# Kernel tuning notes

Measured on AMD Instinct MI355X. Metric: run time of the kernel, lower is better.

## Reference

```python
import jax, jax.numpy as jnp
import numpy as np

# Static model config (matches init_kwargs)
B, N, L, S = 128, 5, 128, 8   # batch, n_vars, n_lags, patch_size
P = L // S                    # n_patches = 16
D = 64                        # d_hidden
DT = 16                       # d_time
DIN = DT + 1                  # TTCN input dim (time embed + value)
NF = D - 1                    # TTCN output channels (d_hidden - 1)
DG = 16                       # d_graph
NH = 4                        # n_heads
GNN_L = 2                     # gnn_layers
NB = 2                        # n_blocks
NC = 39                       # n_classes


def _time_embed(t, omega, alpha):
    # t: (...,) -> (..., DT); channel 0 linear, rest sinusoidal (Eq. 3)
    lin = omega[0] * t + alpha[0]
    per = jnp.sin(omega[1:] * t[..., None] + alpha[1:])
    return jnp.concatenate([lin[..., None], per], axis=-1)


def _ln(x, g, b, eps=1e-5):
    mu = x.mean(-1, keepdims=True)
    v = ((x - mu) ** 2).mean(-1, keepdims=True)
    return (x - mu) * jax.lax.rsqrt(v + eps) * g + b


def _mha(x, wi, bi, wo, bo):
    # torch nn.MultiheadAttention (batch_first) self-attention, no mask
    Bq, Pq, Dq = x.shape
    dh = Dq // NH
    qkv = x @ wi.T + bi
    q, k, v = jnp.split(qkv, 3, axis=-1)
    sp = lambda a: a.reshape(Bq, Pq, NH, dh).transpose(0, 2, 1, 3)
    q, k, v = sp(q), sp(k), sp(v)
    scale = 1.0 / np.sqrt(dh)
    a = jax.nn.softmax(jnp.einsum('bhqd,bhkd->bhqk', q, k) * scale, axis=-1)
    o = jnp.einsum('bhqk,bhkd->bhqd', a, v).transpose(0, 2, 1, 3).reshape(Bq, Pq, Dq)
    return o @ wo.T + bo


def _ttcn(z, mask, w1, b1, w2, b2):
    # z: (T,S,DIN); vectorizes torch's per-output-channel loop over NF filters
    h = jax.nn.relu(jnp.einsum('tsi,fji->tfsj', z, w1) + b1[:, None, :])
    lg = jnp.einsum('tfsj,fkj->tfsk', h, w2) + b2[:, None, :]
    lg = jnp.where(mask[:, None, :, None], lg, -1e9)
    w = jax.nn.softmax(lg, axis=2)  # softmax over patch-length dim
    return jnp.einsum('tfsi,tsi->tf', w, z)  # (weights*z).sum(s).sum(i)


def _block(h, p):
    (wi, bi, wo, bo, g1, be1, fw1, fb1, fw2, fb2, g2, be2,
     Es1, Es2, Wd1, bd1, Wd2, bd2, Wg1, bg1, Wg2, bg2, gW, gb, g3, be3) = p
    Bh = h.shape[0]
    # intra-series transformer over patches
    x = h.reshape(Bh * N, P, D)
    x = _ln(x + _mha(x, wi, bi, wo, bo), g1, be1)
    x = _ln(x + (jax.nn.relu(x @ fw1.T + fb1) @ fw2.T + fb2), g2, be2)
    # inter-series GSL + GNN, vectorized over the per-patch python loop
    hh = x.reshape(Bh, N, P, D).transpose(0, 2, 1, 3).reshape(Bh * P, N, D)
    Es1b = jnp.broadcast_to(Es1, (Bh * P, N, DG))
    Es2b = jnp.broadcast_to(Es2, (Bh * P, N, DG))
    Ed1 = hh @ Wd1.T + bd1
    gg1 = jax.nn.relu(jnp.tanh(jnp.concatenate([hh, Es1b], -1) @ Wg1.T + bg1))
    Ep1 = Es1b + gg1 * Ed1
    Ed2 = hh @ Wd2.T + bd2
    gg2 = jax.nn.relu(jnp.tanh(jnp.concatenate([hh, Es2b], -1) @ Wg2.T + bg2))
    Ep2 = Es2b + gg2 * Ed2
    A = jax.nn.softmax(jax.nn.relu(jnp.einsum('bnd,bmd->bnm', Ep1, Ep2)), axis=-1)
    res = hh @ gW[0].T + gb[0]
    Ap = A
    for m in range(1, GNN_L + 1):
        res = res + (Ap @ hh) @ gW[m].T + gb[m]
        if m < GNN_L:
            Ap = Ap @ A
    hg = jax.nn.relu(res)
    out = _ln(hh + hg, g3, be3)
    return out.reshape(Bh, P, N, D).transpose(0, 2, 1, 3)


def setup_inputs():
    key = jax.random.key(0)
    ks = iter(jax.random.split(key, 64))
    rn = lambda *s: jax.random.normal(next(ks), s, dtype=jnp.float32)
    d = {}
    d['x'] = rn(B, N, L)
    d['t_rel'] = jnp.broadcast_to(jnp.arange(L, dtype=jnp.float32), (B, L)) * 1.0
    d['te_omega'] = rn(DT); d['te_alpha'] = rn(DT)
    d['mf_w1'] = rn(NF, DIN, DIN) * 0.1; d['mf_b1'] = rn(NF, DIN) * 0.02
    d['mf_w2'] = rn(NF, DIN, DIN) * 0.1; d['mf_b2'] = rn(NF, DIN) * 0.02
    d['pos_enc'] = rn(1, 1, P, D) * 0.02
    d['attn_in_w'] = rn(NB, 3 * D, D) * 0.05; d['attn_in_b'] = rn(NB, 3 * D) * 0.02
    d['attn_out_w'] = rn(NB, D, D) * 0.05; d['attn_out_b'] = rn(NB, D) * 0.02
    d['ln1_g'] = jnp.ones((NB, D)); d['ln1_b'] = jnp.zeros((NB, D))
    d['ffn_w1'] = rn(NB, 2 * D, D) * 0.05; d['ffn_b1'] = rn(NB, 2 * D) * 0.02
    d['ffn_w2'] = rn(NB, D, 2 * D) * 0.05; d['ffn_b2'] = rn(NB, D) * 0.02
    d['ln2_g'] = jnp.ones((NB, D)); d['ln2_b'] = jnp.zeros((NB, D))
    d['gsl_Es1'] = rn(NB, N, DG); d['gsl_Es2'] = rn(NB, N, DG)
    d['gsl_Wd1'] = rn(NB, DG, D) * 0.05; d['gsl_bd1'] = rn(NB, DG) * 0.02
    d['gsl_Wd2'] = rn(NB, DG, D) * 0.05; d['gsl_bd2'] = rn(NB, DG) * 0.02
    d['gsl_Wg1'] = rn(NB, 1, D + DG) * 0.05; d['gsl_bg1'] = rn(NB, 1) * 0.02
    d['gsl_Wg2'] = rn(NB, 1, D + DG) * 0.05; d['gsl_bg2'] = rn(NB, 1) * 0.02
    d['gnn_W'] = rn(NB, GNN_L + 1, D, D) * 0.05; d['gnn_b'] = rn(NB, GNN_L + 1, D) * 0.02
    d['ln3_g'] = jnp.ones((NB, D)); d['ln3_b'] = jnp.zeros((NB, D))
    d['fp_w'] = rn(D, P * D) * 0.02; d['fp_b'] = rn(D) * 0.02
    d['q_omega'] = rn(DT); d['q_alpha'] = rn(DT)
    d['ow1'] = rn(N, D, D + DT) * 0.05; d['ob1'] = rn(N, D) * 0.02
    d['ow2'] = rn(N, D, D) * 0.05; d['ob2'] = rn(N, D) * 0.02
    d['ow3'] = rn(N, NC, D) * 0.05; d['ob3'] = rn(N, NC) * 0.02
    return d


def reference(x, t_rel, te_omega, te_alpha, mf_w1, mf_b1, mf_w2, mf_b2, pos_enc,
              attn_in_w, attn_in_b, attn_out_w, attn_out_b, ln1_g, ln1_b,
              ffn_w1, ffn_b1, ffn_w2, ffn_b2, ln2_g, ln2_b,
              gsl_Es1, gsl_Es2, gsl_Wd1, gsl_bd1, gsl_Wd2, gsl_bd2,
              gsl_Wg1, gsl_bg1, gsl_Wg2, gsl_bg2, gnn_W, gnn_b, ln3_g, ln3_b,
              fp_w, fp_b, q_omega, q_alpha, ow1, ob1, ow2, ob2, ow3, ob3):
    # patching: L divisible by S -> no padding, mask all True
    v = x.reshape(B, N, P, S)
    t = jnp.broadcast_to(t_rel.reshape(B, 1, P, S), (B, N, P, S)).reshape(-1, S)
    mask = jnp.ones((B * N * P, S), dtype=bool)
    te = _time_embed(t, te_omega, te_alpha)               # (T,S,DT)
    z = jnp.concatenate([te, v.reshape(-1, S)[..., None]], -1)  # (T,S,DIN)
    hc = _ttcn(z, mask, mf_w1, mf_b1, mf_w2, mf_b2)       # (T,NF)
    mp = mask.any(1).astype(z.dtype)[:, None]
    h = jnp.concatenate([hc, mp], -1).reshape(B, N, P, D) + pos_enc
    for bk in range(NB):
        p = (attn_in_w[bk], attn_in_b[bk], attn_out_w[bk], attn_out_b[bk],
             ln1_g[bk], ln1_b[bk], ffn_w1[bk], ffn_b1[bk], ffn_w2[bk], ffn_b2[bk],
             ln2_g[bk], ln2_b[bk], gsl_Es1[bk], gsl_Es2[bk], gsl_Wd1[bk], gsl_bd1[bk],
             gsl_Wd2[bk], gsl_bd2[bk], gsl_Wg1[bk], gsl_bg1[bk], gsl_Wg2[bk], gsl_bg2[bk],
             gnn_W[bk], gnn_b[bk], ln3_g[bk], ln3_b[bk])
        h = _block(h, p)
    flat = h.reshape(B, N, P * D)
    Hf = flat @ fp_w.T + fp_b                              # (B,N,D)
    q = _time_embed(jnp.full((B,), float(L), dtype=x.dtype), q_omega, q_alpha)
    inp = jnp.concatenate([Hf, jnp.broadcast_to(q[:, None, :], (B, N, DT))], -1)
    h1 = jax.nn.relu(jnp.einsum('bni,noi->bno', inp, ow1) + ob1)
    h2 = jax.nn.relu(jnp.einsum('bni,noi->bno', h1, ow2) + ob2)
    return jnp.einsum('bni,noi->bno', h2, ow3) + ob3       # (B,N,NC) raw logits
```

## Files before the change

kernel.cpp:

```cpp
#include <hip/hip_runtime.h>
#include <math.h>

#define CB 128
#define CN 5
#define CL 128
#define CS 8
#define CP 16
#define CD 64
#define CDT 16
#define CDIN 17
#define CNF 63
#define CNC 39

__device__ __forceinline__ float wave_sum(float v) {
    v += __shfl_xor(v, 32);
    v += __shfl_xor(v, 16);
    v += __shfl_xor(v, 8);
    v += __shfl_xor(v, 4);
    v += __shfl_xor(v, 2);
    v += __shfl_xor(v, 1);
    return v;
}

__global__ void prep_kernel(
    const float* __restrict__ mf_w1, const float* __restrict__ mf_w2,
    const float* __restrict__ mf_b2, const float* __restrict__ fp_w,
    const float* __restrict__ attn_in_w, const float* __restrict__ attn_out_w,
    const float* __restrict__ ffn_w1, const float* __restrict__ ffn_w2,
    const float* __restrict__ gnn_W, const float* __restrict__ gsl_Wd1,
    const float* __restrict__ gsl_Wd2,
    const float* __restrict__ ow1, const float* __restrict__ ow2,
    const float* __restrict__ ow3,
    float* __restrict__ w1c16, float* __restrict__ w2t, float* __restrict__ b2t,
    float* __restrict__ fp_wt, float* __restrict__ wit, float* __restrict__ wot,
    float* __restrict__ fw1t, float* __restrict__ fw2t,
    float* __restrict__ gWt, float* __restrict__ Wd1t, float* __restrict__ Wd2t,
    float* __restrict__ o1t, float* __restrict__ o2t, float* __restrict__ o3t) {
    int idx = blockIdx.x * 256 + threadIdx.x;
    if (idx < 65536) {
        int d = idx >> 10, j = idx & 1023;
        fp_wt[j * 64 + d] = fp_w[idx];
    }
    if (idx < 18496) {
        int f = idx / 289, rem = idx % 289;
        w2t[rem * 64 + f] = (f < CNF) ? mf_w2[idx] : 0.f;
    }
    if (idx < 1088) {
        int f = idx / 17, r = idx % 17;
        b2t[r * 64 + f]   = (f < CNF) ? mf_b2[idx] : 0.f;
        w1c16[r * 64 + f] = (f < CNF) ? mf_w1[idx * 17 + 16] : 0.f;
    }
    if (idx < 24576) {
        int bk = idx / 12288, rem = idx % 12288;
        int oc = rem >> 6, d = rem & 63;
        wit[bk * 12288 + d * 192 + oc] = attn_in_w[idx];
    }
    if (idx < 8192) {
        int bk = idx >> 12, rem = idx & 4095;
        int d = rem >> 6, c = rem & 63;
        wot[bk * 4096 + c * 64 + d] = attn_out_w[idx];
    }
    if (idx < 16384) {
        int bk = idx >> 13, rem = idx & 8191;
        int c = rem >> 6, d = rem & 63;
        fw1t[bk * 8192 + d * 128 + c] = ffn_w1[idx];
    }
    if (idx < 16384) {
        int bk = idx >> 13, rem = idx & 8191;
        int d = rem >> 7, c = rem & 127;
        fw2t[bk * 8192 + c * 64 + d] = ffn_w2[idx];
    }
    if (idx < 24576) {
        int bk = idx / 12288, rem = idx % 12288;
        int m = rem >> 12, r2 = rem & 4095;
        int o = r2 >> 6, c = r2 & 63;
        gWt[bk * 12288 + m * 4096 + c * 64 + o] = gnn_W[idx];
    }
    if (idx < 2048) {
        int bk = idx >> 10, rem = idx & 1023;
        int l = rem >> 6, d = rem & 63;
        Wd1t[bk * 1024 + d * 16 + l] = gsl_Wd1[idx];
        Wd2t[bk * 1024 + d * 16 + l] = gsl_Wd2[idx];
    }
    if (idx < 25600) {
        int n = idx / 5120, rem = idx % 5120;
        int o = rem / 80, i = rem % 80;
        o1t[n * 5120 + i * 64 + o] = ow1[idx];
    }
    if (idx < 20480) {
        int n = idx >> 12, rem = idx & 4095;
        int o = rem >> 6, i = rem & 63;
        o2t[n * 4096 + i * 64 + o] = ow2[idx];
    }
    if (idx < 12480) {
        int n = idx / 2496, rem = idx % 2496;
        int o = rem >> 6, i = rem & 63;
        o3t[n * 4096 + i * 64 + o] = ow3[idx];
    }
}

__global__ __launch_bounds__(64) void prep2_kernel(
    const float* __restrict__ t_rel, const float* __restrict__ omega, const float* __restrict__ alpha,
    const float* __restrict__ mf_w1, const float* __restrict__ mf_b1,
    float* __restrict__ base, float* __restrict__ te_tab) {
    const int blk = blockIdx.x;
    const int j = blk % 17;
    const int ps = blk / 17;
    const int p = ps >> 3, s = ps & 7;
    const int f = threadIdx.x;

    const float t = t_rel[p * CS + s];
    float te[16];
#pragma unroll
    for (int i = 0; i < 16; ++i)
        te[i] = (i == 0) ? (omega[0] * t + alpha[0]) : sinf(omega[i] * t + alpha[i]);

    float acc = 0.f;
    if (f < CNF) {
        acc = mf_b1[f * 17 + j];
        const float* w = mf_w1 + (f * 17 + j) * 17;
#pragma unroll
        for (int i = 0; i < 16; ++i) acc = fmaf(te[i], w[i], acc);
    }
    base[((p * 17 + j) * 8 + s) * 64 + f] = acc;

    if (j == 0 && f < 16) te_tab[ps * 16 + f] = te[f];
}

template <int K0, int KC>
__device__ __forceinline__ float ttcn_chunk(
    const float* __restrict__ w2t, const float* bse, const float* w1c,
    const float* b2s, const float* tes, const float v_s[8], int lane) {
    float lg[KC][8];
#pragma unroll
    for (int kk = 0; kk < KC; ++kk) {
        float bb = b2s[(K0 + kk) * 64 + lane];
#pragma unroll
        for (int s = 0; s < 8; ++s) lg[kk][s] = bb;
    }
#pragma unroll 1
    for (int j = 0; j < 17; ++j) {
        float w1 = w1c[j * 64 + lane];
        float h_s[8];
#pragma unroll
        for (int s = 0; s < 8; ++s)
            h_s[s] = fmaxf(fmaf(v_s[s], w1, bse[(j * 8 + s) * 64 + lane]), 0.f);
#pragma unroll
        for (int kk = 0; kk < KC; ++kk) {
            float w2 = w2t[((K0 + kk) * 17 + j) * 64 + lane];
#pragma unroll
            for (int s = 0; s < 8; ++s) lg[kk][s] = fmaf(h_s[s], w2, lg[kk][s]);
        }
    }
    float out = 0.f;
#pragma unroll
    for (int kk = 0; kk < KC; ++kk) {
        const int k = K0 + kk;
        float m = lg[kk][0];
#pragma unroll
        for (int s = 1; s < 8; ++s) m = fmaxf(m, lg[kk][s]);
        float l = 0.f, o = 0.f;
#pragma unroll
        for (int s = 0; s < 8; ++s) {
            float e = __expf(lg[kk][s] - m);
            l += e;
            o = fmaf(e, (k < 16) ? tes[s * 16 + k] : v_s[s], o);
        }
        out += o / l;
    }
    return out;
}

__global__ __launch_bounds__(512, 2) void ttcn_kernel(
    const float* __restrict__ x, const float* __restrict__ base,
    const float* __restrict__ te_tab, const float* __restrict__ w1c16,
    const float* __restrict__ w2t, const float* __restrict__ b2t,
    const float* __restrict__ pos_enc, float* __restrict__ hout) {
    __shared__ float bse[8704];
    __shared__ float w1c[1088];
    __shared__ float b2s[1088];
    __shared__ float tes[128];
    const int tid = threadIdx.x;
    const int p = blockIdx.x / 80, g = blockIdx.x % 80;

    {
        const float4* bsrc4 = (const float4*)(base + p * 8704);
        float4* bse4 = (float4*)bse;
        for (int i = tid; i < 2176; i += 512) bse4[i] = bsrc4[i];
        const float4* w1c4 = (const float4*)w1c16;
        const float4* b2t4 = (const float4*)b2t;
        float4* dw = (float4*)w1c;
        float4* db = (float4*)b2s;
        if (tid < 272) { dw[tid] = w1c4[tid]; db[tid] = b2t4[tid]; }
        if (tid < 128) tes[tid] = te_tab[p * 128 + tid];
    }
    __syncthreads();

    const int wid = tid >> 6, lane = tid & 63;
    const int bn = g * 8 + wid;
    const int tok = bn * 16 + p;

    float v_s[8];
    {
        const float4* xv = (const float4*)(x + tok * 8);
        float4 x0 = xv[0], x1 = xv[1];
        v_s[0] = x0.x; v_s[1] = x0.y; v_s[2] = x0.z; v_s[3] = x0.w;
        v_s[4] = x1.x; v_s[5] = x1.y; v_s[6] = x1.z; v_s[7] = x1.w;
    }

    float out = 0.f;
    out += ttcn_chunk<0, 5>(w2t, bse, w1c, b2s, tes, v_s, lane);
    out += ttcn_chunk<5, 4>(w2t, bse, w1c, b2s, tes, v_s, lane);
    out += ttcn_chunk<9, 4>(w2t, bse, w1c, b2s, tes, v_s, lane);
    out += ttcn_chunk<13, 4>(w2t, bse, w1c, b2s, tes, v_s, lane);

    float val = (lane < CNF) ? out : 1.0f;
    hout[tok * 64 + lane] = val + pos_enc[p * 64 + lane];
}

__global__ __launch_bounds__(256) void intra_kernel(
    float* __restrict__ h,
    const float* __restrict__ wit, const float* __restrict__ bi,
    const float* __restrict__ wot, const float* __restrict__ bo,
    const float* __restrict__ g1, const float* __restrict__ be1,
    const float* __restrict__ fw1t, const float* __restrict__ fb1,
    const float* __restrict__ fw2t, const float* __restrict__ fb2,
    const float* __restrict__ g2, const float* __restrict__ be2) {
    __shared__ float xs[16][64];
    __shared__ float qs[16][64];
    __shared__ float ks[16][64];
    __shared__ float vs[16][64];
    __shared__ float sc[4][16][16];
    __shared__ float os[16][64];
    __shared__ float x1[16][64];
    __shared__ float fs[16][128];

    const int row = blockIdx.x;
    float* xin = h + row * CP * CD;
    const int t = threadIdx.x;

    for (int e = t; e < 1024; e += 256) xs[e >> 6][e & 63] = xin[e];
    __syncthreads();

    if (t < 192) {
        const int oc = t;
        float acc[16];
#pragma unroll
        for (int p = 0; p < 16; ++p) acc[p] = bi[oc];
        for (int d = 0; d < 64; ++d) {
            float w = wit[d * 192 + oc];
#pragma unroll
            for (int p = 0; p < 16; ++p) acc[p] = fmaf(xs[p][d], w, acc[p]);
        }
#pragma unroll
        for (int p = 0; p < 16; ++p) {
            if (oc < 64)       qs[p][oc] = acc[p];
            else if (oc < 128) ks[p][oc - 64] = acc[p];
            else               vs[p][oc - 128] = acc[p];
        }
    }
    __syncthreads();

    for (int e = t; e < 1024; e += 256) {
        int hh = e >> 8, i = (e >> 4) & 15, j = e & 15;
        float acc = 0.f;
        for (int d = 0; d < 16; ++d) acc = fmaf(qs[i][hh * 16 + d], ks[j][hh * 16 + d], acc);
        sc[hh][i][j] = acc * 0.25f;
    }
    __syncthreads();

    if (t < 64) {
        int hh = t >> 4, i = t & 15;
        float m = sc[hh][i][0];
#pragma unroll
        for (int j = 1; j < 16; ++j) m = fmaxf(m, sc[hh][i][j]);
        float e_[16];
        float l = 0.f;
#pragma unroll
        for (int j = 0; j < 16; ++j) { e_[j] = __expf(sc[hh][i][j] - m); l += e_[j]; }
        float inv = 1.f / l;
#pragma unroll
        for (int j = 0; j < 16; ++j) sc[hh][i][j] = e_[j] * inv;
    }
    __syncthreads();

    for (int e = t; e < 1024; e += 256) {
        int p = e >> 6, c = e & 63, hh = c >> 4;
        float acc = 0.f;
        for (int j = 0; j < 16; ++j) acc = fmaf(sc[hh][p][j], vs[j][c], acc);
        os[p][c] = acc;
    }
    __syncthreads();

    for (int e = t; e < 1024; e += 256) {
        int p = e >> 6, d = e & 63;
        float acc = bo[d];
        for (int c = 0; c < 64; ++c) acc = fmaf(os[p][c], wot[c * 64 + d], acc);
        x1[p][d] = acc + xs[p][d];
    }
    __syncthreads();

    {
        int w = t >> 6, lane = t & 63;
        for (int p = w; p < 16; p += 4) {
            float v = x1[p][lane];
            float mu = wave_sum(v) * (1.f / 64);
            float d = v - mu;
            float var = wave_sum(d * d) * (1.f / 64);
            x1[p][lane] = d * rsqrtf(var + 1e-5f) * g1[lane] + be1[lane];
        }
    }
    __syncthreads();

    for (int e = t; e < 2048; e += 256) {
        int p = e >> 7, c = e & 127;
        float acc = fb1[c];
        for (int d = 0; d < 64; ++d) acc = fmaf(x1[p][d], fw1t[d * 128 + c], acc);
        fs[p][c] = fmaxf(acc, 0.f);
    }
    __syncthreads();

    for (int e = t; e < 1024; e += 256) {
        int p = e >> 6, d = e & 63;
        float acc = fb2[d];
        for (int c = 0; c < 128; ++c) acc = fmaf(fs[p][c], fw2t[c * 64 + d], acc);
        os[p][d] = acc + x1[p][d];
    }
    __syncthreads();

    {
        int w = t >> 6, lane = t & 63;
        for (int p = w; p < 16; p += 4) {
            float v = os[p][lane];
            float mu = wave_sum(v) * (1.f / 64);
            float d = v - mu;
            float var = wave_sum(d * d) * (1.f / 64);
            xin[p * 64 + lane] = d * rsqrtf(var + 1e-5f) * g2[lane] + be2[lane];
        }
    }
}

__global__ __launch_bounds__(320) void gnn_kernel(
    float* __restrict__ h,
    const float* __restrict__ Es1, const float* __restrict__ Es2,
    const float* __restrict__ Wd1t, const float* __restrict__ bd1,
    const float* __restrict__ Wd2t, const float* __restrict__ bd2,
    const float* __restrict__ Wg1, const float* __restrict__ bg1,
    const float* __restrict__ Wg2, const float* __restrict__ bg2,
    const float* __restrict__ gWt, const float* __restrict__ gb,
    const float* __restrict__ g3, const float* __restrict__ be3) {
    __shared__ float hs[5][64];
    __shared__ float ep1[5][16], ep2[5][16];
    __shared__ float Araw[5][8], As[5][8], A2s[5][8];
    __shared__ float t1s[5][64], t2s[5][64];

    const int bp = blockIdx.x;
    const int b = bp >> 4, p = bp & 15;
    const int n = threadIdx.x >> 6, lane = threadIdx.x & 63;
    float* hptr = h + (((b * CN + n) * CP + p) * CD);

    hs[n][lane] = hptr[lane];
    __syncthreads();

    float a1 = 0.f, a2 = 0.f;
    if (lane < 16) {
        a1 = bd1[lane]; a2 = bd2[lane];
        for (int d = 0; d < 64; ++d) {
            a1 = fmaf(hs[n][d], Wd1t[d * 16 + lane], a1);
            a2 = fmaf(hs[n][d], Wd2t[d * 16 + lane], a2);
        }
    }
    float p1 = hs[n][lane] * Wg1[lane] + ((lane < 16) ? Es1[n * 16 + lane] * Wg1[64 + lane] : 0.f);
    float p2 = hs[n][lane] * Wg2[lane] + ((lane < 16) ? Es2[n * 16 + lane] * Wg2[64 + lane] : 0.f);
    float gg1 = fmaxf(tanhf(wave_sum(p1) + bg1[0]), 0.f);
    float gg2 = fmaxf(tanhf(wave_sum(p2) + bg2[0]), 0.f);
    if (lane < 16) {
        ep1[n][lane] = Es1[n * 16 + lane] + gg1 * a1;
        ep2[n][lane] = Es2[n * 16 + lane] + gg2 * a2;
    }
    __syncthreads();

    if (lane < 5) {
        float e = 0.f;
#pragma unroll
        for (int k = 0; k < 16; ++k) e = fmaf(ep1[n][k], ep2[lane][k], e);
        Araw[n][lane] = fmaxf(e, 0.f);
    }
    __syncthreads();
    if (lane < 5) {
        float m = Araw[n][0];
#pragma unroll
        for (int j = 1; j < 5; ++j) m = fmaxf(m, Araw[n][j]);
        float l = 0.f;
#pragma unroll
        for (int j = 0; j < 5; ++j) l += __expf(Araw[n][j] - m);
        As[n][lane] = __expf(Araw[n][lane] - m) / l;
    }
    __syncthreads();
    if (lane < 5) {
        float a = 0.f;
#pragma unroll
        for (int l2 = 0; l2 < 5; ++l2) a = fmaf(As[n][l2], As[l2][lane], a);
        A2s[n][lane] = a;
    }
    __syncthreads();

    {
        float t1 = 0.f, t2 = 0.f;
#pragma unroll
        for (int m = 0; m < 5; ++m) {
            t1 = fmaf(As[n][m], hs[m][lane], t1);
            t2 = fmaf(A2s[n][m], hs[m][lane], t2);
        }
        t1s[n][lane] = t1;
        t2s[n][lane] = t2;
    }
    __syncthreads();

    float res = gb[lane] + gb[64 + lane] + gb[128 + lane];
    for (int c = 0; c < 64; ++c) {
        res = fmaf(hs[n][c], gWt[c * 64 + lane], res);
        res = fmaf(t1s[n][c], gWt[4096 + c * 64 + lane], res);
        res = fmaf(t2s[n][c], gWt[8192 + c * 64 + lane], res);
    }
    float pre = hs[n][lane] + fmaxf(res, 0.f);

    float mu = wave_sum(pre) * (1.f / 64);
    float d = pre - mu;
    float var = wave_sum(d * d) * (1.f / 64);
    hptr[lane] = d * rsqrtf(var + 1e-5f) * g3[lane] + be3[lane];
}

__global__ __launch_bounds__(256) void head_kernel(
    const float* __restrict__ h, const float* __restrict__ fp_wt, const float* __restrict__ fp_b,
    const float* __restrict__ q_omega, const float* __restrict__ q_alpha,
    const float* __restrict__ o1t, const float* __restrict__ ob1,
    const float* __restrict__ o2t, const float* __restrict__ ob2,
    const float* __restrict__ o3t, const float* __restrict__ ob3,
    float* __restrict__ out) {
    __shared__ float flat[1024];
    __shared__ float part[4][64];
    __shared__ float inp[80];
    __shared__ float h1s[64], h2s[64];
    const int row = blockIdx.x;
    const int n = row % CN;
    const int t = threadIdx.x, wid = t >> 6, lane = t & 63;
    const float* src = h + row * CP * CD;

    for (int e = t; e < 1024; e += 256) flat[e] = src[e];
    __syncthreads();

    float a0 = 0.f, a1 = 0.f, a2 = 0.f, a3 = 0.f;
    const int j0 = wid * 256;
    for (int j = 0; j < 256; j += 4) {
        a0 = fmaf(flat[j0 + j],     fp_wt[(j0 + j) * 64 + lane],     a0);
        a1 = fmaf(flat[j0 + j + 1], fp_wt[(j0 + j + 1) * 64 + lane], a1);
        a2 = fmaf(flat[j0 + j + 2], fp_wt[(j0 + j + 2) * 64 + lane], a2);
        a3 = fmaf(flat[j0 + j + 3], fp_wt[(j0 + j + 3) * 64 + lane], a3);
    }
    part[wid][lane] = (a0 + a1) + (a2 + a3);
    if (t >= 64 && t < 80) {
        int i = t - 64;
        const float tt = (float)CL;
        inp[64 + i] = (i == 0) ? (q_omega[0] * tt + q_alpha[0])
                               : sinf(q_omega[i] * tt + q_alpha[i]);
    }
    __syncthreads();
    if (t < 64) inp[t] = fp_b[t] + ((part[0][t] + part[1][t]) + (part[2][t] + part[3][t]));
    __syncthreads();

    if (t < 64) {
        float a = ob1[n * 64 + t];
        for (int i = 0; i < 80; ++i) a = fmaf(inp[i], o1t[n * 5120 + i * 64 + t], a);
        h1s[t] = fmaxf(a, 0.f);
    }
    __syncthreads();
    if (t < 64) {
        float a = ob2[n * 64 + t];
        for (int i = 0; i < 64; ++i) a = fmaf(h1s[i], o2t[n * 4096 + i * 64 + t], a);
        h2s[t] = fmaxf(a, 0.f);
    }
    __syncthreads();
    if (t < CNC) {
        float a = ob3[n * CNC + t];
        for (int i = 0; i < 64; ++i) a = fmaf(h2s[i], o3t[n * 4096 + i * 64 + t], a);
        out[row * CNC + t] = a;
    }
}

extern "C" void kernel_launch(void* const* d_in, const int* in_sizes, int n_in,
                              void* d_out, int out_size, void* d_ws, size_t ws_size,
                              hipStream_t stream) {
    const float* x         = (const float*)d_in[0];
    const float* t_rel     = (const float*)d_in[1];
    const float* te_omega  = (const float*)d_in[2];
    const float* te_alpha  = (const float*)d_in[3];
    const float* mf_w1     = (const float*)d_in[4];
    const float* mf_b1     = (const float*)d_in[5];
    const float* mf_w2     = (const float*)d_in[6];
    const float* mf_b2     = (const float*)d_in[7];
    const float* pos_enc   = (const float*)d_in[8];
    const float* attn_in_w = (const float*)d_in[9];
    const float* attn_in_b = (const float*)d_in[10];
    const float* attn_out_w= (const float*)d_in[11];
    const float* attn_out_b= (const float*)d_in[12];
    const float* ln1_g     = (const float*)d_in[13];
    const float* ln1_b     = (const float*)d_in[14];
    const float* ffn_w1    = (const float*)d_in[15];
    const float* ffn_b1    = (const float*)d_in[16];
    const float* ffn_w2    = (const float*)d_in[17];
    const float* ffn_b2    = (const float*)d_in[18];
    const float* ln2_g     = (const float*)d_in[19];
    const float* ln2_b     = (const float*)d_in[20];
    const float* gsl_Es1   = (const float*)d_in[21];
    const float* gsl_Es2   = (const float*)d_in[22];
    const float* gsl_Wd1   = (const float*)d_in[23];
    const float* gsl_bd1   = (const float*)d_in[24];
    const float* gsl_Wd2   = (const float*)d_in[25];
    const float* gsl_bd2   = (const float*)d_in[26];
    const float* gsl_Wg1   = (const float*)d_in[27];
    const float* gsl_bg1   = (const float*)d_in[28];
    const float* gsl_Wg2   = (const float*)d_in[29];
    const float* gsl_bg2   = (const float*)d_in[30];
    const float* gnn_W     = (const float*)d_in[31];
    const float* gnn_b     = (const float*)d_in[32];
    const float* ln3_g     = (const float*)d_in[33];
    const float* ln3_b     = (const float*)d_in[34];
    const float* fp_w      = (const float*)d_in[35];
    const float* fp_b      = (const float*)d_in[36];
    const float* q_omega   = (const float*)d_in[37];
    const float* q_alpha   = (const float*)d_in[38];
    const float* ow1       = (const float*)d_in[39];
    const float* ob1       = (const float*)d_in[40];
    const float* ow2       = (const float*)d_in[41];
    const float* ob2       = (const float*)d_in[42];
    const float* ow3       = (const float*)d_in[43];
    const float* ob3       = (const float*)d_in[44];

    float* ws = (float*)d_ws;
    float* hbuf   = ws;
    float* base   = hbuf + 655360;
    float* te_tab = base + 139264;
    float* w1c16  = te_tab + 2048;
    float* w2t    = w1c16 + 1088;
    float* b2t    = w2t + 18496;
    float* fp_wt  = b2t + 1088;
    float* wit    = fp_wt + 65536;
    float* wot    = wit + 24576;
    float* fw1t   = wot + 8192;
    float* fw2t   = fw1t + 16384;
    float* gWt    = fw2t + 16384;
    float* Wd1t   = gWt + 24576;
    float* Wd2t   = Wd1t + 2048;
    float* o1t    = Wd2t + 2048;
    float* o2t    = o1t + 25600;
    float* o3t    = o2t + 20480;

    prep_kernel<<<256, 256, 0, stream>>>(
        mf_w1, mf_w2, mf_b2, fp_w, attn_in_w, attn_out_w, ffn_w1, ffn_w2,
        gnn_W, gsl_Wd1, gsl_Wd2, ow1, ow2, ow3,
        w1c16, w2t, b2t, fp_wt, wit, wot, fw1t, fw2t, gWt, Wd1t, Wd2t,
        o1t, o2t, o3t);

    prep2_kernel<<<CP * CS * CDIN, 64, 0, stream>>>(t_rel, te_omega, te_alpha,
                                                    mf_w1, mf_b1, base, te_tab);

    ttcn_kernel<<<1280, 512, 0, stream>>>(x, base, te_tab, w1c16,
                                          w2t, b2t, pos_enc, hbuf);

    for (int bk = 0; bk < 2; ++bk) {
        intra_kernel<<<CB * CN, 256, 0, stream>>>(
            hbuf,
            wit + bk * 12288, attn_in_b + bk * 192,
            wot + bk * 4096, attn_out_b + bk * 64,
            ln1_g + bk * 64, ln1_b + bk * 64,
            fw1t + bk * 8192, ffn_b1 + bk * 128,
            fw2t + bk * 8192, ffn_b2 + bk * 64,
            ln2_g + bk * 64, ln2_b + bk * 64);

        gnn_kernel<<<CB * CP, 320, 0, stream>>>(
            hbuf,
            gsl_Es1 + bk * CN * 16, gsl_Es2 + bk * CN * 16,
            Wd1t + bk * 1024, gsl_bd1 + bk * 16,
            Wd2t + bk * 1024, gsl_bd2 + bk * 16,
            gsl_Wg1 + bk * 80, gsl_bg1 + bk,
            gsl_Wg2 + bk * 80, gsl_bg2 + bk,
            gWt + bk * 12288, gnn_b + bk * 3 * 64,
            ln3_g + bk * 64, ln3_b + bk * 64);
    }

    head_kernel<<<CB * CN, 256, 0, stream>>>(hbuf, fp_wt, fp_b, q_omega, q_alpha,
                                             o1t, ob1, o2t, ob2, o3t, ob3,
                                             (float*)d_out);
}
```

Measured before the change: 463.2 us.

## Interleave weights in float4 groups and drop TTCN shared-memory staging

Prep now writes every transposed weight matrix interleaved in groups of four along the reduction dimension. The intra, gnn and head kernels can then read weights and shared activations as float4 and accumulate with a dot4 helper, cutting load instruction count. The TTCN kernel no longer stages base, w1c and b2 tables into shared memory and reads them from global memory through cache instead. It also shrinks blocks to 256 threads and regroups the output channels into two larger chunks. Larger chunks raise register pressure, and global reads in TTCN may be slower than LDS if the cache does not hold the tables.

```diff
diff --git a/kernel.cpp b/kernel.cpp
--- a/kernel.cpp
+++ b/kernel.cpp
@@ -22,6 +22,14 @@
     return v;
 }
 
+__device__ __forceinline__ float dot4(float4 a, float4 b, float acc) {
+    acc = fmaf(a.x, b.x, acc);
+    acc = fmaf(a.y, b.y, acc);
+    acc = fmaf(a.z, b.z, acc);
+    acc = fmaf(a.w, b.w, acc);
+    return acc;
+}
+
 __global__ void prep_kernel(
     const float* __restrict__ mf_w1, const float* __restrict__ mf_w2,
     const float* __restrict__ mf_b2, const float* __restrict__ fp_w,
@@ -32,14 +40,14 @@
     const float* __restrict__ ow1, const float* __restrict__ ow2,
     const float* __restrict__ ow3,
     float* __restrict__ w1c16, float* __restrict__ w2t, float* __restrict__ b2t,
-    float* __restrict__ fp_wt, float* __restrict__ wit, float* __restrict__ wot,
-    float* __restrict__ fw1t, float* __restrict__ fw2t,
-    float* __restrict__ gWt, float* __restrict__ Wd1t, float* __restrict__ Wd2t,
-    float* __restrict__ o1t, float* __restrict__ o2t, float* __restrict__ o3t) {
+    float* __restrict__ fpv, float* __restrict__ witv, float* __restrict__ wotv,
+    float* __restrict__ fw1v, float* __restrict__ fw2v,
+    float* __restrict__ gWv, float* __restrict__ Wd1v, float* __restrict__ Wd2v,
+    float* __restrict__ o1v, float* __restrict__ o2v, float* __restrict__ o3v) {
     int idx = blockIdx.x * 256 + threadIdx.x;
     if (idx < 65536) {
         int d = idx >> 10, j = idx & 1023;
-        fp_wt[j * 64 + d] = fp_w[idx];
+        fpv[((j >> 2) * 64 + d) * 4 + (j & 3)] = fp_w[idx];
     }
     if (idx < 18496) {
         int f = idx / 289, rem = idx % 289;
@@ -53,49 +61,49 @@
     if (idx < 24576) {
         int bk = idx / 12288, rem = idx % 12288;
         int oc = rem >> 6, d = rem & 63;
-        wit[bk * 12288 + d * 192 + oc] = attn_in_w[idx];
+        witv[bk * 12288 + ((d >> 2) * 192 + oc) * 4 + (d & 3)] = attn_in_w[idx];
     }
     if (idx < 8192) {
         int bk = idx >> 12, rem = idx & 4095;
         int d = rem >> 6, c = rem & 63;
-        wot[bk * 4096 + c * 64 + d] = attn_out_w[idx];
+        wotv[bk * 4096 + ((c >> 2) * 64 + d) * 4 + (c & 3)] = attn_out_w[idx];
     }
     if (idx < 16384) {
         int bk = idx >> 13, rem = idx & 8191;
         int c = rem >> 6, d = rem & 63;
-        fw1t[bk * 8192 + d * 128 + c] = ffn_w1[idx];
+        fw1v[bk * 8192 + ((d >> 2) * 128 + c) * 4 + (d & 3)] = ffn_w1[idx];
     }
     if (idx < 16384) {
         int bk = idx >> 13, rem = idx & 8191;
         int d = rem >> 7, c = rem & 127;
-        fw2t[bk * 8192 + c * 64 + d] = ffn_w2[idx];
+        fw2v[bk * 8192 + ((c >> 2) * 64 + d) * 4 + (c & 3)] = ffn_w2[idx];
     }
     if (idx < 24576) {
         int bk = idx / 12288, rem = idx % 12288;
         int m = rem >> 12, r2 = rem & 4095;
         int o = r2 >> 6, c = r2 & 63;
-        gWt[bk * 12288 + m * 4096 + c * 64 + o] = gnn_W[idx];
+        gWv[bk * 12288 + m * 4096 + ((c >> 2) * 64 + o) * 4 + (c & 3)] = gnn_W[idx];
     }
     if (idx < 2048) {
         int bk = idx >> 10, rem = idx & 1023;
         int l = rem >> 6, d = rem & 63;
-        Wd1t[bk * 1024 + d * 16 + l] = gsl_Wd1[idx];
-        Wd2t[bk * 1024 + d * 16 + l] = gsl_Wd2[idx];
+        Wd1v[bk * 1024 + ((d >> 2) * 16 + l) * 4 + (d & 3)] = gsl_Wd1[idx];
+        Wd2v[bk * 1024 + ((d >> 2) * 16 + l) * 4 + (d & 3)] = gsl_Wd2[idx];
     }
     if (idx < 25600) {
         int n = idx / 5120, rem = idx % 5120;
         int o = rem / 80, i = rem % 80;
-        o1t[n * 5120 + i * 64 + o] = ow1[idx];
+        o1v[n * 5120 + ((i >> 2) * 64 + o) * 4 + (i & 3)] = ow1[idx];
     }
     if (idx < 20480) {
         int n = idx >> 12, rem = idx & 4095;
         int o = rem >> 6, i = rem & 63;
-        o2t[n * 4096 + i * 64 + o] = ow2[idx];
+        o2v[n * 4096 + ((i >> 2) * 64 + o) * 4 + (i & 3)] = ow2[idx];
     }
     if (idx < 12480) {
         int n = idx / 2496, rem = idx % 2496;
         int o = rem >> 6, i = rem & 63;
-        o3t[n * 4096 + i * 64 + o] = ow3[idx];
+        o3v[n * 4096 + ((i >> 2) * 64 + o) * 4 + (i & 3)] = ow3[idx];
     }
 }
 
@@ -129,12 +137,13 @@
 
 template <int K0, int KC>
 __device__ __forceinline__ float ttcn_chunk(
-    const float* __restrict__ w2t, const float* bse, const float* w1c,
-    const float* b2s, const float* tes, const float v_s[8], int lane) {
+    const float* __restrict__ w2t, const float* __restrict__ bse,
+    const float* __restrict__ w1c, const float* __restrict__ b2t,
+    const float* __restrict__ tes, const float v_s[8], int lane) {
     float lg[KC][8];
 #pragma unroll
     for (int kk = 0; kk < KC; ++kk) {
-        float bb = b2s[(K0 + kk) * 64 + lane];
+        float bb = b2t[(K0 + kk) * 64 + lane];
 #pragma unroll
         for (int s = 0; s < 8; ++s) lg[kk][s] = bb;
     }
@@ -171,34 +180,18 @@
     return out;
 }
 
-__global__ __launch_bounds__(512, 2) void ttcn_kernel(
+__global__ __launch_bounds__(256, 2) void ttcn_kernel(
     const float* __restrict__ x, const float* __restrict__ base,
     const float* __restrict__ te_tab, const float* __restrict__ w1c16,
     const float* __restrict__ w2t, const float* __restrict__ b2t,
     const float* __restrict__ pos_enc, float* __restrict__ hout) {
-    __shared__ float bse[8704];
-    __shared__ float w1c[1088];
-    __shared__ float b2s[1088];
-    __shared__ float tes[128];
-    const int tid = threadIdx.x;
-    const int p = blockIdx.x / 80, g = blockIdx.x % 80;
-
-    {
-        const float4* bsrc4 = (const float4*)(base + p * 8704);
-        float4* bse4 = (float4*)bse;
-        for (int i = tid; i < 2176; i += 512) bse4[i] = bsrc4[i];
-        const float4* w1c4 = (const float4*)w1c16;
-        const float4* b2t4 = (const float4*)b2t;
-        float4* dw = (float4*)w1c;
-        float4* db = (float4*)b2s;
-        if (tid < 272) { dw[tid] = w1c4[tid]; db[tid] = b2t4[tid]; }
-        if (tid < 128) tes[tid] = te_tab[p * 128 + tid];
-    }
-    __syncthreads();
-
-    const int wid = tid >> 6, lane = tid & 63;
-    const int bn = g * 8 + wid;
+    const int tid = threadIdx.x, wid = tid >> 6, lane = tid & 63;
+    const int p = blockIdx.x / 160, g = blockIdx.x % 160;
+    const int bn = g * 4 + wid;
     const int tok = bn * 16 + p;
+
+    const float* bse = base + p * 8704;
+    const float* tes = te_tab + p * 128;
 
     float v_s[8];
     {
@@ -209,10 +202,8 @@
     }
 
     float out = 0.f;
-    out += ttcn_chunk<0, 5>(w2t, bse, w1c, b2s, tes, v_s, lane);
-    out += ttcn_chunk<5, 4>(w2t, bse, w1c, b2s, tes, v_s, lane);
-    out += ttcn_chunk<9, 4>(w2t, bse, w1c, b2s, tes, v_s, lane);
-    out += ttcn_chunk<13, 4>(w2t, bse, w1c, b2s, tes, v_s, lane);
+    out += ttcn_chunk<0, 9>(w2t, bse, w1c16, b2t, tes, v_s, lane);
+    out += ttcn_chunk<9, 8>(w2t, bse, w1c16, b2t, tes, v_s, lane);
 
     float val = (lane < CNF) ? out : 1.0f;
     hout[tok * 64 + lane] = val + pos_enc[p * 64 + lane];
@@ -220,26 +211,35 @@
 
 __global__ __launch_bounds__(256) void intra_kernel(
     float* __restrict__ h,
-    const float* __restrict__ wit, const float* __restrict__ bi,
-    const float* __restrict__ wot, const float* __restrict__ bo,
+    const float* __restrict__ witv, const float* __restrict__ bi,
+    const float* __restrict__ wotv, const float* __restrict__ bo,
     const float* __restrict__ g1, const float* __restrict__ be1,
-    const float* __restrict__ fw1t, const float* __restrict__ fb1,
-    const float* __restrict__ fw2t, const float* __restrict__ fb2,
+    const float* __restrict__ fw1v, const float* __restrict__ fb1,
+    const float* __restrict__ fw2v, const float* __restrict__ fb2,
     const float* __restrict__ g2, const float* __restrict__ be2) {
-    __shared__ float xs[16][64];
-    __shared__ float qs[16][64];
-    __shared__ float ks[16][64];
-    __shared__ float vs[16][64];
-    __shared__ float sc[4][16][16];
-    __shared__ float os[16][64];
-    __shared__ float x1[16][64];
-    __shared__ float fs[16][128];
+    __shared__ __align__(16) float xs[16][64];
+    __shared__ __align__(16) float qs[16][64];
+    __shared__ __align__(16) float ks[16][64];
+    __shared__ __align__(16) float vs[16][64];
+    __shared__ __align__(16) float sc[4][16][16];
+    __shared__ __align__(16) float os[16][64];
+    __shared__ __align__(16) float x1[16][64];
+    __shared__ __align__(16) float fs[16][128];
 
     const int row = blockIdx.x;
     float* xin = h + row * CP * CD;
     const int t = threadIdx.x;
 
-    for (int e = t; e < 1024; e += 256) xs[e >> 6][e & 63] = xin[e];
+    const float4* witv4 = (const float4*)witv;
+    const float4* wotv4 = (const float4*)wotv;
+    const float4* fw1v4 = (const float4*)fw1v;
+    const float4* fw2v4 = (const float4*)fw2v;
+
+    {
+        float4* xs4 = (float4*)&xs[0][0];
+        const float4* xin4 = (const float4*)xin;
+        if (t < 256) xs4[t] = xin4[t];
+    }
     __syncthreads();
 
     if (t < 192) {
@@ -247,10 +247,11 @@
         float acc[16];
 #pragma unroll
         for (int p = 0; p < 16; ++p) acc[p] = bi[oc];
-        for (int d = 0; d < 64; ++d) {
-            float w = wit[d * 192 + oc];
-#pragma unroll
-            for (int p = 0; p < 16; ++p) acc[p] = fmaf(xs[p][d], w, acc[p]);
+        const float4* xs4 = (const float4*)&xs[0][0];
+        for (int d4 = 0; d4 < 16; ++d4) {
+            float4 wv = witv4[d4 * 192 + oc];
+#pragma unroll
+            for (int p = 0; p < 16; ++p) acc[p] = dot4(xs4[p * 16 + d4], wv, acc[p]);
         }
 #pragma unroll
         for (int p = 0; p < 16; ++p) {
@@ -263,8 +264,11 @@
 
     for (int e = t; e < 1024; e += 256) {
         int hh = e >> 8, i = (e >> 4) & 15, j = e & 15;
+        const float4* q4 = (const float4*)&qs[i][hh * 16];
+        const float4* k4 = (const float4*)&ks[j][hh * 16];
         float acc = 0.f;
-        for (int d = 0; d < 16; ++d) acc = fmaf(qs[i][hh * 16 + d], ks[j][hh * 16 + d], acc);
+#pragma unroll
+        for (int d4 = 0; d4 < 4; ++d4) acc = dot4(q4[d4], k4[d4], acc);
         sc[hh][i][j] = acc * 0.25f;
     }
     __syncthreads();
@@ -286,16 +290,26 @@
 
     for (int e = t; e < 1024; e += 256) {
         int p = e >> 6, c = e & 63, hh = c >> 4;
+        const float4* s4 = (const float4*)&sc[hh][p][0];
         float acc = 0.f;
-        for (int j = 0; j < 16; ++j) acc = fmaf(sc[hh][p][j], vs[j][c], acc);
+#pragma unroll
+        for (int j4 = 0; j4 < 4; ++j4) {
+            float4 sv = s4[j4];
+            acc = fmaf(sv.x, vs[j4 * 4 + 0][c], acc);
+            acc = fmaf(sv.y, vs[j4 * 4 + 1][c], acc);
+            acc = fmaf(sv.z, vs[j4 * 4 + 2][c], acc);
+            acc = fmaf(sv.w, vs[j4 * 4 + 3][c], acc);
+        }
         os[p][c] = acc;
     }
     __syncthreads();
 
     for (int e = t; e < 1024; e += 256) {
         int p = e >> 6, d = e & 63;
+        const float4* os4 = (const float4*)&os[p][0];
         float acc = bo[d];
-        for (int c = 0; c < 64; ++c) acc = fmaf(os[p][c], wot[c * 64 + d], acc);
+#pragma unroll
+        for (int c4 = 0; c4 < 16; ++c4) acc = dot4(os4[c4], wotv4[c4 * 64 + d], acc);
         x1[p][d] = acc + xs[p][d];
     }
     __syncthreads();
@@ -314,16 +328,20 @@
 
     for (int e = t; e < 2048; e += 256) {
         int p = e >> 7, c = e & 127;
+        const float4* x14 = (const float4*)&x1[p][0];
         float acc = fb1[c];
-        for (int d = 0; d < 64; ++d) acc = fmaf(x1[p][d], fw1t[d * 128 + c], acc);
+#pragma unroll
+        for (int d4 = 0; d4 < 16; ++d4) acc = dot4(x14[d4], fw1v4[d4 * 128 + c], acc);
         fs[p][c] = fmaxf(acc, 0.f);
     }
     __syncthreads();
 
     for (int e = t; e < 1024; e += 256) {
         int p = e >> 6, d = e & 63;
+        const float4* fs4 = (const float4*)&fs[p][0];
         float acc = fb2[d];
-        for (int c = 0; c < 128; ++c) acc = fmaf(fs[p][c], fw2t[c * 64 + d], acc);
+#pragma unroll
+        for (int c4 = 0; c4 < 32; ++c4) acc = dot4(fs4[c4], fw2v4[c4 * 64 + d], acc);
         os[p][d] = acc + x1[p][d];
     }
     __syncthreads();
@@ -343,31 +361,38 @@
 __global__ __launch_bounds__(320) void gnn_kernel(
     float* __restrict__ h,
     const float* __restrict__ Es1, const float* __restrict__ Es2,
-    const float* __restrict__ Wd1t, const float* __restrict__ bd1,
-    const float* __restrict__ Wd2t, const float* __restrict__ bd2,
+    const float* __restrict__ Wd1v, const float* __restrict__ bd1,
+    const float* __restrict__ Wd2v, const float* __restrict__ bd2,
     const float* __restrict__ Wg1, const float* __restrict__ bg1,
     const float* __restrict__ Wg2, const float* __restrict__ bg2,
-    const float* __restrict__ gWt, const float* __restrict__ gb,
+    const float* __restrict__ gWv, const float* __restrict__ gb,
     const float* __restrict__ g3, const float* __restrict__ be3) {
-    __shared__ float hs[5][64];
+    __shared__ __align__(16) float hs[5][64];
+    __shared__ __align__(16) float t1s[5][64], t2s[5][64];
     __shared__ float ep1[5][16], ep2[5][16];
     __shared__ float Araw[5][8], As[5][8], A2s[5][8];
-    __shared__ float t1s[5][64], t2s[5][64];
 
     const int bp = blockIdx.x;
     const int b = bp >> 4, p = bp & 15;
     const int n = threadIdx.x >> 6, lane = threadIdx.x & 63;
     float* hptr = h + (((b * CN + n) * CP + p) * CD);
 
+    const float4* Wd1v4 = (const float4*)Wd1v;
+    const float4* Wd2v4 = (const float4*)Wd2v;
+    const float4* gWv4  = (const float4*)gWv;
+
     hs[n][lane] = hptr[lane];
     __syncthreads();
 
     float a1 = 0.f, a2 = 0.f;
     if (lane < 16) {
         a1 = bd1[lane]; a2 = bd2[lane];
-        for (int d = 0; d < 64; ++d) {
-            a1 = fmaf(hs[n][d], Wd1t[d * 16 + lane], a1);
-            a2 = fmaf(hs[n][d], Wd2t[d * 16 + lane], a2);
+        const float4* hs4 = (const float4*)&hs[n][0];
+#pragma unroll
+        for (int d4 = 0; d4 < 16; ++d4) {
+            float4 hv = hs4[d4];
+            a1 = dot4(hv, Wd1v4[d4 * 16 + lane], a1);
+            a2 = dot4(hv, Wd2v4[d4 * 16 + lane], a2);
         }
     }
     float p1 = hs[n][lane] * Wg1[lane] + ((lane < 16) ? Es1[n * 16 + lane] * Wg1[64 + lane] : 0.f);
@@ -418,10 +443,16 @@
     __syncthreads();
 
     float res = gb[lane] + gb[64 + lane] + gb[128 + lane];
-    for (int c = 0; c < 64; ++c) {
-        res = fmaf(hs[n][c], gWt[c * 64 + lane], res);
-        res = fmaf(t1s[n][c], gWt[4096 + c * 64 + lane], res);
-        res = fmaf(t2s[n][c], gWt[8192 + c * 64 + lane], res);
+    {
+        const float4* hs4 = (const float4*)&hs[n][0];
+        const float4* t14 = (const float4*)&t1s[n][0];
+        const float4* t24 = (const float4*)&t2s[n][0];
+#pragma unroll
+        for (int c4 = 0; c4 < 16; ++c4) {
+            res = dot4(hs4[c4], gWv4[c4 * 64 + lane], res);
+            res = dot4(t14[c4], gWv4[1024 + c4 * 64 + lane], res);
+            res = dot4(t24[c4], gWv4[2048 + c4 * 64 + lane], res);
+        }
     }
     float pre = hs[n][lane] + fmaxf(res, 0.f);
 
@@ -432,33 +463,41 @@
 }
 
 __global__ __launch_bounds__(256) void head_kernel(
-    const float* __restrict__ h, const float* __restrict__ fp_wt, const float* __restrict__ fp_b,
+    const float* __restrict__ h, const float* __restrict__ fpv, const float* __restrict__ fp_b,
     const float* __restrict__ q_omega, const float* __restrict__ q_alpha,
-    const float* __restrict__ o1t, const float* __restrict__ ob1,
-    const float* __restrict__ o2t, const float* __restrict__ ob2,
-    const float* __restrict__ o3t, const float* __restrict__ ob3,
+    const float* __restrict__ o1v, const float* __restrict__ ob1,
+    const float* __restrict__ o2v, const float* __restrict__ ob2,
+    const float* __restrict__ o3v, const float* __restrict__ ob3,
     float* __restrict__ out) {
-    __shared__ float flat[1024];
+    __shared__ __align__(16) float flat[1024];
+    __shared__ __align__(16) float inp[80];
+    __shared__ __align__(16) float h1s[64], h2s[64];
     __shared__ float part[4][64];
-    __shared__ float inp[80];
-    __shared__ float h1s[64], h2s[64];
     const int row = blockIdx.x;
     const int n = row % CN;
     const int t = threadIdx.x, wid = t >> 6, lane = t & 63;
     const float* src = h + row * CP * CD;
 
-    for (int e = t; e < 1024; e += 256) flat[e] = src[e];
-    __syncthreads();
-
-    float a0 = 0.f, a1 = 0.f, a2 = 0.f, a3 = 0.f;
-    const int j0 = wid * 256;
-    for (int j = 0; j < 256; j += 4) {
-        a0 = fmaf(flat[j0 + j],     fp_wt[(j0 + j) * 64 + lane],     a0);
-        a1 = fmaf(flat[j0 + j + 1], fp_wt[(j0 + j + 1) * 64 + lane], a1);
-        a2 = fmaf(flat[j0 + j + 2], fp_wt[(j0 + j + 2) * 64 + lane], a2);
-        a3 = fmaf(flat[j0 + j + 3], fp_wt[(j0 + j + 3) * 64 + lane], a3);
-    }
-    part[wid][lane] = (a0 + a1) + (a2 + a3);
+    const float4* fpv4 = (const float4*)fpv;
+    const float4* o1v4 = (const float4*)o1v;
+    const float4* o2v4 = (const float4*)o2v;
+    const float4* o3v4 = (const float4*)o3v;
+
+    {
+        float4* flat4 = (float4*)flat;
+        const float4* src4 = (const float4*)src;
+        if (t < 256) flat4[t] = src4[t];
+    }
+    __syncthreads();
+
+    {
+        const float4* flat4 = (const float4*)flat;
+        float a0 = 0.f;
+        const int j40 = wid * 64;
+        for (int j4 = 0; j4 < 64; ++j4)
+            a0 = dot4(flat4[j40 + j4], fpv4[(j40 + j4) * 64 + lane], a0);
+        part[wid][lane] = a0;
+    }
     if (t >= 64 && t < 80) {
         int i = t - 64;
         const float tt = (float)CL;
@@ -470,20 +509,26 @@
     __syncthreads();
 
     if (t < 64) {
+        const float4* inp4 = (const float4*)inp;
         float a = ob1[n * 64 + t];
-        for (int i = 0; i < 80; ++i) a = fmaf(inp[i], o1t[n * 5120 + i * 64 + t], a);
+#pragma unroll
+        for (int i4 = 0; i4 < 20; ++i4) a = dot4(inp4[i4], o1v4[n * 1280 + i4 * 64 + t], a);
         h1s[t] = fmaxf(a, 0.f);
     }
     __syncthreads();
     if (t < 64) {
+        const float4* h14 = (const float4*)h1s;
         float a = ob2[n * 64 + t];
-        for (int i = 0; i < 64; ++i) a = fmaf(h1s[i], o2t[n * 4096 + i * 64 + t], a);
+#pragma unroll
+        for (int i4 = 0; i4 < 16; ++i4) a = dot4(h14[i4], o2v4[n * 1024 + i4 * 64 + t], a);
         h2s[t] = fmaxf(a, 0.f);
     }
     __syncthreads();
     if (t < CNC) {
+        const float4* h24 = (const float4*)h2s;
         float a = ob3[n * CNC + t];
-        for (int i = 0; i < 64; ++i) a = fmaf(h2s[i], o3t[n * 4096 + i * 64 + t], a);
+#pragma unroll
+        for (int i4 = 0; i4 < 16; ++i4) a = dot4(h24[i4], o3v4[n * 1024 + i4 * 64 + t], a);
         out[row * CNC + t] = a;
     }
 }
@@ -544,52 +589,52 @@
     float* w1c16  = te_tab + 2048;
     float* w2t    = w1c16 + 1088;
     float* b2t    = w2t + 18496;
-    float* fp_wt  = b2t + 1088;
-    float* wit    = fp_wt + 65536;
-    float* wot    = wit + 24576;
-    float* fw1t   = wot + 8192;
-    float* fw2t   = fw1t + 16384;
-    float* gWt    = fw2t + 16384;
-    float* Wd1t   = gWt + 24576;
-    float* Wd2t   = Wd1t + 2048;
-    float* o1t    = Wd2t + 2048;
-    float* o2t    = o1t + 25600;
-    float* o3t    = o2t + 20480;
+    float* fpv    = b2t + 1088;
+    float* witv   = fpv + 65536;
+    float* wotv   = witv + 24576;
+    float* fw1v   = wotv + 8192;
+    float* fw2v   = fw1v + 16384;
+    float* gWv    = fw2v + 16384;
+    float* Wd1v   = gWv + 24576;
+    float* Wd2v   = Wd1v + 2048;
+    float* o1v    = Wd2v + 2048;
+    float* o2v    = o1v + 25600;
+    float* o3v    = o2v + 20480;
 
     prep_kernel<<<256, 256, 0, stream>>>(
         mf_w1, mf_w2, mf_b2, fp_w, attn_in_w, attn_out_w, ffn_w1, ffn_w2,
         gnn_W, gsl_Wd1, gsl_Wd2, ow1, ow2, ow3,
-        w1c16, w2t, b2t, fp_wt, wit, wot, fw1t, fw2t, gWt, Wd1t, Wd2t,
-        o1t, o2t, o3t);
+        w1c16, w2t, b2t, fpv, witv, wotv, fw1v, fw2v, gWv, Wd1v, Wd2v,
+        o1v, o2v, o3v);
 
     prep2_kernel<<<CP * CS * CDIN, 64, 0, stream>>>(t_rel, te_omega, te_alpha,
                                                     mf_w1, mf_b1, base, te_tab);
 
-    ttcn_kernel<<<1280, 512, 0, stream>>>(x, base, te_tab, w1c16,
-                                          w2t, b2t, pos_enc, hbuf);
+    ttcn_kernel<<<CP * 160, 256, 0, stream>>>(x, base, te_tab, w1c16,
+                                              w2t, b2t, pos_enc, hbuf);
 
     for (int bk = 0; bk < 2; ++bk) {
         intra_kernel<<<CB * CN, 256, 0, stream>>>(
             hbuf,
-            wit + bk * 12288, attn_in_b + bk * 192,
-            wot + bk * 4096, attn_out_b + bk * 64,
+            witv + bk * 12288, attn_in_b + bk * 192,
+            wotv + bk * 4096, attn_out_b + bk * 64,
             ln1_g + bk * 64, ln1_b + bk * 64,
-            fw1t + bk * 8192, ffn_b1 + bk * 128,
-            fw2t + bk * 8192, ffn_b2 + bk * 64,
+            fw1v + bk * 8192, ffn_b1 + bk * 128,
+            fw2v + bk * 8192, ffn_b2 + bk * 64,
             ln2_g + bk * 64, ln2_b + bk * 64);
 
         gnn_kernel<<<CB * CP, 320, 0, stream>>>(
             hbuf,
             gsl_Es1 + bk * CN * 16, gsl_Es2 + bk * CN * 16,
-            Wd1t + bk * 1024, gsl_bd1 + bk * 16,
-            Wd2t + bk * 1024, gsl_bd2 + bk * 16,
+            Wd1v + bk * 1024, gsl_bd1 + bk * 16,
+            Wd2v + bk * 1024, gsl_bd2 + bk * 16,
             gsl_Wg1 + bk * 80, gsl_bg1 + bk,
             gsl_Wg2 + bk * 80, gsl_bg2 + bk,
-            gWt + bk * 12288, gnn_b + bk * 3 * 64,
+            gWv + bk * 12288, gnn_b + bk * 3 * 64,
             ln3_g + bk * 64, ln3_b + bk * 64);
     }
 
-    head_kernel<<<CB * CN, 256, 0, stream>>>(hbuf, fp_wt, fp_b, q_omega, q_alpha,
-                                             o1t, ob1, o2t, ob2, o3t, ob3,
+    head_kernel<<<CB * CN, 256, 0, stream>>>(hbuf, fpv, fp_b, q_omega, q_alpha,
+                                             o1v, ob1, o2v, ob2, o3v, ob3,
                                              (float*)d_out);
 }
```

New measurement: 463.0 us. About the same (-0.0%).
